# Kernel tuning notes

Hardware: AMD Instinct MI355X
Metric: run time of the kernel (lower is better)

The kernel has to match this reference:

```python
import jax, jax.numpy as jnp
import numpy as np

HID = 1024
RATIO = 4          # compress_ratio
SELECT_K = 512
WINDOW = 256
N_HEADS = 16
SCALE = 1.0 / np.sqrt(HID // N_HEADS)  # 1/sqrt(head_size), head_size=64


def setup_inputs() -> dict:
    key = jax.random.key(0)
    ks = jax.random.split(key, 12)
    std = 0.02
    d = {
        "hidden_states": jax.random.normal(ks[0], (4, 4096, HID), jnp.float32),
        # torch Linear weight [out,in] stored here transposed as [in,out]
        "Wq": jax.random.normal(ks[1], (HID, HID), jnp.float32) * std,
        "bq": jnp.zeros((HID,), jnp.float32),
        "Wk": jax.random.normal(ks[2], (HID, HID), jnp.float32) * std,
        "bk": jnp.zeros((HID,), jnp.float32),
        "Wv": jax.random.normal(ks[3], (HID, HID), jnp.float32) * std,
        "bv": jnp.zeros((HID,), jnp.float32),
        "Wo": jax.random.normal(ks[4], (3 * HID, HID), jnp.float32) * std,
        "bo": jnp.zeros((HID,), jnp.float32),
        "Wg": jax.random.normal(ks[5], (HID, 3), jnp.float32) * std,
        "bg": jnp.zeros((3,), jnp.float32),
        "Wc": jax.random.normal(ks[6], (RATIO * HID, HID), jnp.float32) * std,
        "bc": jnp.zeros((HID,), jnp.float32),
        "Ws": jax.random.normal(ks[7], (HID, 1), jnp.float32) * std,
        "bs": jnp.zeros((1,), jnp.float32),
    }
    return d


def _adjust(t, L):
    cur = t.shape[1]
    if cur < L:
        return jnp.pad(t, ((0, 0), (0, L - cur), (0, 0)))
    return t[:, :L]


def _attend(x, Wq, bq, Wk, bk, Wv, bv):
    # x: [..., T, H]; full single-head attention over axis -2
    q = x @ Wq + bq
    k = x @ Wk + bk
    v = x @ Wv + bv
    s = jnp.einsum('...qd,...kd->...qk', q, k) * SCALE
    p = jax.nn.softmax(s, axis=-1)
    return jnp.einsum('...qk,...kd->...qd', p, v)


def reference(hidden_states, Wq, bq, Wk, bk, Wv, bv, Wo, bo, Wg, bg, Wc, bc, Ws, bs):
    B, L, H = hidden_states.shape

    # --- gates ---
    gates = jax.nn.sigmoid(hidden_states @ Wg + bg)
    gates = gates / (gates.sum(-1, keepdims=True) + 1e-6)

    # --- compress branch: block-compress then full attention over blocks ---
    pad_c = (-L) % RATIO
    xc = jnp.pad(hidden_states, ((0, 0), (0, pad_c), (0, 0)))
    blocks = xc.reshape(B, -1, RATIO * H)
    compressed = blocks @ Wc + bc                      # [B, Lc, H]
    comp_out = _adjust(_attend(compressed, Wq, bq, Wk, bk, Wv, bv), L)

    # --- select branch: top-k token gather then full attention ---
    k_eff = min(SELECT_K, L)
    scores = (hidden_states @ Ws + bs)[..., 0]         # [B, L]
    _, idx = jax.lax.top_k(scores, k_eff)
    idx = jnp.sort(idx, axis=-1)
    selected = jnp.take_along_axis(hidden_states, idx[..., None], axis=1)  # [B, k, H]
    sel_out = _adjust(_attend(selected, Wq, bq, Wk, bk, Wv, bv), L)

    # --- window branch: overlapping sliding windows (stride W/2) ---
    W = min(WINDOW, L)
    pad_w = (-L) % W
    xw = jnp.pad(hidden_states, ((0, 0), (0, pad_w), (0, 0)))
    Lp = xw.shape[1]
    starts = np.arange(0, Lp - W + 1, W // 2)
    widx = starts[:, None] + np.arange(W)              # [nw, W] static
    win = xw[:, widx]                                   # [B, nw, W, H]
    win_ctx = _attend(win, Wq, bq, Wk, bk, Wv, bv)      # [B, nw, W, H]
    win_out = _adjust(win_ctx.reshape(B, -1, H), L)

    # --- gated combine + output projection + residual + layernorm ---
    combined = jnp.concatenate([
        comp_out * gates[..., 0:1],
        sel_out * gates[..., 1:2],
        win_out * gates[..., 2:3],
    ], axis=-1)
    out = combined @ Wo + bo
    out = out * 0.5 + hidden_states * 0.5
    mu = out.mean(-1, keepdims=True)
    var = out.var(-1, keepdims=True)
    return (out - mu) * jax.lax.rsqrt(var + 1e-6)
```

## Files before the change

kernel.cpp:

```cpp
#include <hip/hip_runtime.h>
#include <hip/hip_bf16.h>

typedef __bf16 bf16;
typedef __bf16 bf16x4 __attribute__((ext_vector_type(4)));
typedef __bf16 bf16x8 __attribute__((ext_vector_type(8)));
typedef float floatx4 __attribute__((ext_vector_type(4)));

#define MFMA16(a, b, c) __builtin_amdgcn_mfma_f32_16x16x32_bf16((a), (b), (c), 0, 0, 0)
#define SCALE_F 0.125f

#define GLDS(gp, lp) __builtin_amdgcn_global_load_lds( \
    (const __attribute__((address_space(1))) void*)(gp), \
    (__attribute__((address_space(3))) void*)(lp), 16, 0, 0)

__global__ __launch_bounds__(256) void prep_kernel(const float* __restrict__ Wq, const float* __restrict__ Wk,
                                                   const float* __restrict__ Wv, const float* __restrict__ Wo,
                                                   const float* __restrict__ Wc,
                                                   const float* __restrict__ bq, const float* __restrict__ bk,
                                                   const float* __restrict__ bv,
                                                   bf16* __restrict__ wqkvT, bf16* __restrict__ woT,
                                                   bf16* __restrict__ wcT, float* __restrict__ bqkv) {
    const int z = blockIdx.z;
    const int tx = threadIdx.x, ty = threadIdx.y;
    if (z == 10) {
        int bid = blockIdx.y * 32 + blockIdx.x;
        if (bid < 12) {
            int i = bid * 256 + ty * 32 + tx;
            float v = (i < 1024) ? bq[i] : (i < 2048 ? bk[i - 1024] : bv[i - 2048]);
            bqkv[i] = v;
        }
        return;
    }
    __shared__ float tile[32][33];
    const float* in;
    bf16* out;
    int R;
    if (z < 3)      { in = (z == 0 ? Wq : (z == 1 ? Wk : Wv)); out = wqkvT + (size_t)z * 1048576; R = 1024; }
    else if (z < 6) { in = Wo + (size_t)(z - 3) * 1048576; out = woT + (size_t)(z - 3) * 1048576; R = 1024; }
    else            { in = Wc + (size_t)(z - 6) * 1048576; out = wcT + (z - 6) * 1024; R = 4096; }
    int bx = blockIdx.x * 32, by = blockIdx.y * 32;
#pragma unroll
    for (int i = 0; i < 32; i += 8)
        tile[ty + i][tx] = in[(size_t)(by + ty + i) * 1024 + bx + tx];
    __syncthreads();
#pragma unroll
    for (int i = 0; i < 32; i += 8)
        out[(size_t)(bx + ty + i) * R + by + tx] = (bf16)tile[tx][ty + i];
}

__global__ __launch_bounds__(256) void gates_scores_kernel(const float* __restrict__ x,
                                                           const float* __restrict__ Wg, const float* __restrict__ bg,
                                                           const float* __restrict__ Ws, const float* __restrict__ bs,
                                                           float* __restrict__ gates, float* __restrict__ scores,
                                                           bf16* __restrict__ xb) {
    int row = blockIdx.x * 4 + (threadIdx.x >> 6);
    int lane = threadIdx.x & 63;
    const float* xr = x + (size_t)row * 1024 + lane * 16;
    float g0 = 0.f, g1 = 0.f, g2 = 0.f;
    double sc = 0.0;
    bf16x8 xo0, xo1;
#pragma unroll
    for (int i = 0; i < 16; i++) {
        float xv = xr[i];
        if (i < 8) xo0[i] = (bf16)xv; else xo1[i - 8] = (bf16)xv;
        int k = lane * 16 + i;
        g0 += xv * Wg[k * 3 + 0];
        g1 += xv * Wg[k * 3 + 1];
        g2 += xv * Wg[k * 3 + 2];
        sc += (double)(xv * Ws[k]);
    }
    bf16* xbp = xb + (size_t)row * 1024 + lane * 16;
    *(bf16x8*)xbp = xo0;
    *(bf16x8*)(xbp + 8) = xo1;
    for (int off = 1; off < 64; off <<= 1) {
        g0 += __shfl_xor(g0, off);
        g1 += __shfl_xor(g1, off);
        g2 += __shfl_xor(g2, off);
        sc += __shfl_xor(sc, off);
    }
    if (lane == 0) {
        g0 = 1.0f / (1.0f + __expf(-(g0 + bg[0])));
        g1 = 1.0f / (1.0f + __expf(-(g1 + bg[1])));
        g2 = 1.0f / (1.0f + __expf(-(g2 + bg[2])));
        float den = g0 + g1 + g2 + 1e-6f;
        gates[(size_t)row * 3 + 0] = g0 / den;
        gates[(size_t)row * 3 + 1] = g1 / den;
        gates[(size_t)row * 3 + 2] = g2 / den;
        scores[row] = (float)(sc + (double)bs[0]);
    }
}

__global__ __launch_bounds__(256) void rank_kernel(const float* __restrict__ scores, int* __restrict__ rankP) {
    __shared__ float s[1024];
    const int b = blockIdx.z, jc = blockIdx.y;
    const int i = blockIdx.x * 256 + threadIdx.x;
    const float* sb = scores + b * 4096;
    ((float4*)s)[threadIdx.x] = ((const float4*)(sb + jc * 1024))[threadIdx.x];
    __syncthreads();
    const float si = sb[i];
    const int jbase = jc * 1024;
    int cnt = 0;
#pragma unroll 4
    for (int jj = 0; jj < 1024; jj += 4) {
        float4 v = *(const float4*)(s + jj);
        int j0 = jbase + jj;
        cnt += (v.x > si) || (v.x == si && (j0 + 0) < i);
        cnt += (v.y > si) || (v.y == si && (j0 + 1) < i);
        cnt += (v.z > si) || (v.z == si && (j0 + 2) < i);
        cnt += (v.w > si) || (v.w == si && (j0 + 3) < i);
    }
    rankP[jc * 16384 + b * 4096 + i] = cnt;
}

__global__ __launch_bounds__(1024) void select_kernel(const int* __restrict__ rankP, int* __restrict__ sidx) {
    __shared__ int psum[1024];
    int b = blockIdx.x, t = threadIdx.x;
    const int* rb = rankP + b * 4096;
    int f[4];
#pragma unroll
    for (int k = 0; k < 4; k++) {
        int idx = 4 * t + k;
        int r = rb[idx] + rb[16384 + idx] + rb[32768 + idx] + rb[49152 + idx];
        f[k] = r < 512;
    }
    psum[t] = f[0] + f[1] + f[2] + f[3];
    __syncthreads();
    for (int off = 1; off < 1024; off <<= 1) {
        int u = (t >= off) ? psum[t - off] : 0;
        __syncthreads();
        psum[t] += u;
        __syncthreads();
    }
    int pos = t ? psum[t - 1] : 0;
    int* ob = sidx + b * 512;
    if (f[0]) ob[pos++] = 4 * t + 0;
    if (f[1]) ob[pos++] = 4 * t + 1;
    if (f[2]) ob[pos++] = 4 * t + 2;
    if (f[3]) ob[pos++] = 4 * t + 3;
}

__global__ __launch_bounds__(256) void gather_kernel(const bf16* __restrict__ Qf, const bf16* __restrict__ Kf,
                                                     const bf16* __restrict__ Vf, const int* __restrict__ sidx,
                                                     bf16* __restrict__ sq, bf16* __restrict__ sk,
                                                     bf16* __restrict__ sv) {
    int e = blockIdx.x * 256 + threadIdx.x;
    int col = (e & 127) * 8;
    int i = (e >> 7) & 511;
    int b = e >> 16;
    int src = b * 4096 + (sidx[b * 512 + i] & 4095);
    size_t so = (size_t)src * 1024 + col;
    size_t dofs = (size_t)(b * 512 + i) * 1024 + col;
    *(float4*)(sq + dofs) = *(const float4*)(Qf + so);
    *(float4*)(sk + dofs) = *(const float4*)(Kf + so);
    *(float4*)(sv + dofs) = *(const float4*)(Vf + so);
}

__global__ __launch_bounds__(256) void addcvt4_kernel(const float* __restrict__ P0, const float* __restrict__ P1,
                                                      const float* __restrict__ P2, const float* __restrict__ P3,
                                                      const float* __restrict__ bc, bf16* __restrict__ outp) {
    int i = blockIdx.x * 256 + threadIdx.x;
    float4 a = ((const float4*)P0)[i];
    float4 b = ((const float4*)P1)[i];
    float4 c = ((const float4*)P2)[i];
    float4 d = ((const float4*)P3)[i];
    int col = (i << 2) & 1023;
    bf16x4 o;
    o[0] = (bf16)(a.x + b.x + c.x + d.x + bc[col + 0]);
    o[1] = (bf16)(a.y + b.y + c.y + d.y + bc[col + 1]);
    o[2] = (bf16)(a.z + b.z + c.z + d.z + bc[col + 2]);
    o[3] = (bf16)(a.w + b.w + c.w + d.w + bc[col + 3]);
    *(bf16x4*)(outp + ((size_t)i << 2)) = o;
}

template <bool F32OUT, bool ACC, bool REMAP>
__device__ __forceinline__ void gemm3_body(int nt, int mt, int zh, int zl, bf16* sA, bf16* sB,
                                           const bf16* __restrict__ A, const bf16* __restrict__ Bt,
                                           void* __restrict__ Cv, const float* __restrict__ bias, int biasz,
                                           int K, int lda, int ldb, int ldc,
                                           size_t sAhi, size_t sAlo, size_t sBhi, size_t sBlo,
                                           size_t sChi, size_t sClo, int mpbA, int mpbC) {
    const int t = threadIdx.x;
    const int lane = t & 63, quad = lane >> 4, l16 = lane & 15;
    const int wv = t >> 6, wm = wv >> 1, wn = wv & 1;
    A  += (size_t)zh * sAhi + (size_t)zl * sAlo;
    Bt += (size_t)zh * sBhi + (size_t)zl * sBlo;
    const size_t cofs = (size_t)zh * sChi + (size_t)zl * sClo;

    floatx4 acc[4][4] = {};

    const bf16* Ap = A + (size_t)(mt * 128 + (t >> 2)) * lda + (t & 3) * 8;
    const bf16* Bp = Bt + (size_t)(nt * 128 + (t >> 2)) * ldb + (t & 3) * 8;
    const size_t rA = (size_t)64 * lda, rB = (size_t)64 * ldb;
    bf16* lA0 = sA + wv * 512;
    bf16* lA1 = sA + 2048 + wv * 512;
    bf16* lB0 = sB + wv * 512;
    bf16* lB1 = sB + 2048 + wv * 512;

    for (int k0 = 0; k0 < K; k0 += 32) {
        __syncthreads();
        GLDS(Ap + k0,      lA0);
        GLDS(Ap + rA + k0, lA1);
        GLDS(Bp + k0,      lB0);
        GLDS(Bp + rB + k0, lB1);
        __syncthreads();
        bf16x8 af[4], bfr[4];
#pragma unroll
        for (int i = 0; i < 4; i++) af[i] = *(const bf16x8*)(sA + (wm * 64 + i * 16 + l16) * 32 + quad * 8);
#pragma unroll
        for (int j = 0; j < 4; j++) bfr[j] = *(const bf16x8*)(sB + (wn * 64 + j * 16 + l16) * 32 + quad * 8);
#pragma unroll
        for (int i = 0; i < 4; i++)
#pragma unroll
            for (int j = 0; j < 4; j++) acc[i][j] = MFMA16(af[i], bfr[j], acc[i][j]);
    }

#pragma unroll
    for (int i = 0; i < 4; i++) {
        int gr0 = mt * 128 + wm * 64 + i * 16 + quad * 4;
#pragma unroll
        for (int j = 0; j < 4; j++) {
            int gc = nt * 128 + wn * 64 + j * 16 + l16;
            float bvl = bias ? bias[zl * biasz + gc] : 0.0f;
#pragma unroll
            for (int r = 0; r < 4; r++) {
                int row = gr0 + r;
                size_t crow = REMAP ? ((size_t)(row / mpbA) * mpbC + (row % mpbA)) : (size_t)row;
                size_t off = cofs + crow * ldc + gc;
                float v = acc[i][j][r] + bvl;
                if constexpr (F32OUT) {
                    float* Cf = (float*)Cv;
                    if constexpr (ACC) v += Cf[off];
                    Cf[off] = v;
                } else {
                    bf16* Cb = (bf16*)Cv;
                    if constexpr (ACC) v += (float)Cb[off];
                    Cb[off] = (bf16)v;
                }
            }
        }
    }
}

template <bool NZF, bool F32OUT, bool ACC, bool REMAP>
__global__ __launch_bounds__(256) void gemm3(const bf16* __restrict__ A, const bf16* __restrict__ Bt,
                                             void* __restrict__ Cv, const float* __restrict__ bias, int biasz,
                                             int K, int lda, int ldb, int ldc, int zdiv,
                                             size_t sAhi, size_t sAlo, size_t sBhi, size_t sBlo,
                                             size_t sChi, size_t sClo, int mpbA, int mpbC) {
    __shared__ float4 smA[512], smB[512];
    const int mt = blockIdx.y;
    int nt, zh, zl;
    if constexpr (NZF) {
        zh = blockIdx.z;
        zl = blockIdx.x / zdiv;
        nt = blockIdx.x - zl * zdiv;
    } else {
        nt = blockIdx.x;
        int z = blockIdx.z;
        zh = z / zdiv;
        zl = z - zh * zdiv;
    }
    gemm3_body<F32OUT, ACC, REMAP>(nt, mt, zh, zl, (bf16*)smA, (bf16*)smB,
                                   A, Bt, Cv, bias, biasz, K, lda, ldb, ldc,
                                   sAhi, sAlo, sBhi, sBlo, sChi, sClo, mpbA, mpbC);
}

template <bool F32OUT>
__global__ __launch_bounds__(256) void gemm3_pair(int nzA, int nxB, int nyB,
        const bf16* __restrict__ A1, const bf16* __restrict__ B1, void* __restrict__ C1,
        int K1, int lda1, int ldb1, int ldc1, size_t sAhi1, size_t sBhi1, size_t sChi1,
        const bf16* __restrict__ A2, const bf16* __restrict__ B2, void* __restrict__ C2,
        int K2, int lda2, int ldb2, int ldc2, size_t sAhi2, size_t sBhi2, size_t sChi2) {
    __shared__ float4 smA[512], smB[512];
    if ((int)blockIdx.z < nzA) {
        gemm3_body<F32OUT, false, false>(blockIdx.x, blockIdx.y, blockIdx.z, 0, (bf16*)smA, (bf16*)smB,
                                         A1, B1, C1, nullptr, 0, K1, lda1, ldb1, ldc1,
                                         sAhi1, 0, sBhi1, 0, sChi1, 0, 1, 1);
    } else {
        if ((int)blockIdx.x >= nxB || (int)blockIdx.y >= nyB) return;
        gemm3_body<F32OUT, false, false>(blockIdx.x, blockIdx.y, blockIdx.z - nzA, 0, (bf16*)smA, (bf16*)smB,
                                         A2, B2, C2, nullptr, 0, K2, lda2, ldb2, ldc2,
                                         sAhi2, 0, sBhi2, 0, sChi2, 0, 1, 1);
    }
}

#define BARx()   asm volatile("s_barrier" ::: "memory")
#define LGKM0()  asm volatile("s_waitcnt lgkmcnt(0)" ::: "memory")
#define VMC6()   asm volatile("s_waitcnt vmcnt(6)" ::: "memory")

#define LD_A(bsel, qm) { \
    const bf16* _p = lds + (bsel) * 32768 + (((qm) << 7) + (wm << 6) + l16) * 64; \
    _Pragma("unroll") \
    for (int m = 0; m < 4; m++) { \
        a[m][0] = *(const bf16x8*)(_p + (m << 10) + cg0); \
        a[m][1] = *(const bf16x8*)(_p + (m << 10) + cg1); \
    } }

#define LD_B(bsel, qn) { \
    const bf16* _p = lds + (bsel) * 32768 + 16384 + (((qn) << 7) + (wn << 5) + l16) * 64; \
    _Pragma("unroll") \
    for (int n = 0; n < 2; n++) { \
        b[qn][n][0] = *(const bf16x8*)(_p + (n << 10) + cg0); \
        b[qn][n][1] = *(const bf16x8*)(_p + (n << 10) + cg1); \
    } }

#define ST_A(bsel, h, ko) { \
    bf16* _d = lds + (bsel) * 32768 + (((h) << 7) + (wv << 3)) * 64; \
    const bf16* _g = Ab + (size_t)((h) << 7) * lda + (ko); \
    GLDS(_g, _d); \
    GLDS(_g + ((size_t)lda << 6), _d + 4096); }

#define ST_B(bsel, h, ko) { \
    bf16* _d = lds + (bsel) * 32768 + 16384 + (((h) << 7) + (wv << 3)) * 64; \
    const bf16* _g = Bb + (size_t)((h) << 7) * ldb + (ko); \
    GLDS(_g, _d); \
    GLDS(_g + ((size_t)ldb << 6), _d + 4096); }

#define PH_MMA(qm, qn) { \
    __builtin_amdgcn_s_setprio(1); \
    _Pragma("unroll") \
    for (int kk = 0; kk < 2; kk++) \
    _Pragma("unroll") \
    for (int m = 0; m < 4; m++) \
    _Pragma("unroll") \
    for (int n = 0; n < 2; n++) \
        acc[qm][qn][m][n] = MFMA16(a[m][kk], b[qn][n][kk], acc[qm][qn][m][n]); \
    __builtin_amdgcn_s_setprio(0); }

template <bool NZF, bool F32OUT, bool ACC, bool REMAP>
__global__ __launch_bounds__(512, 2) void gemm256(const bf16* __restrict__ A, const bf16* __restrict__ Bt,
                                                  void* __restrict__ Cv, const float* __restrict__ bias, int biasz,
                                                  int K, int lda, int ldb, int ldc, int zdiv,
                                                  size_t sAhi, size_t sAlo, size_t sBhi, size_t sBlo,
                                                  size_t sChi, size_t sClo, int mpbA, int mpbC) {
    __shared__ float4 ldsv[8192];
    bf16* lds = (bf16*)ldsv;
    const int t = threadIdx.x;
    const int lane = t & 63, quad = lane >> 4, l16 = lane & 15;
    const int wv = t >> 6, wm = wv >> 2, wn = wv & 3;

    const int gx = gridDim.x;
    int lin = blockIdx.x + gx * blockIdx.y;
    const int chunk = (gx * gridDim.y) >> 3;
    lin = (lin & 7) * chunk + (lin >> 3);
    const int bx = lin % gx;
    const int mt = lin / gx;

    int nt, zh, zl;
    if constexpr (NZF) {
        zh = blockIdx.z;
        zl = bx / zdiv;
        nt = bx - zl * zdiv;
    } else {
        nt = bx;
        int z = blockIdx.z;
        zh = z / zdiv;
        zl = z - zh * zdiv;
    }
    A  += (size_t)zh * sAhi + (size_t)zl * sAlo;
    Bt += (size_t)zh * sBhi + (size_t)zl * sBlo;
    const size_t cofs = (size_t)zh * sChi + (size_t)zl * sClo;

    const int srow = (wv << 3) + (lane >> 3);
    const int scol = (((lane & 7) ^ ((lane >> 3) & 7)) << 3);
    const bf16* Ab = A + (size_t)(mt * 256 + srow) * lda + scol;
    const bf16* Bb = Bt + (size_t)(nt * 256 + srow) * ldb + scol;
    const int swz = l16 & 7;
    const int cg0 = ((quad ^ swz) << 3);
    const int cg1 = (((4 | quad) ^ swz) << 3);

    floatx4 acc[2][2][4][2] = {};
    bf16x8 a[4][2], b[2][2][2];

    const int NT = K >> 6;
    ST_A(0, 0, 0);  ST_B(0, 0, 0);  ST_B(0, 1, 0);  ST_A(0, 1, 0);
    ST_A(1, 0, 64); ST_B(1, 0, 64); ST_B(1, 1, 64); ST_A(1, 1, 64);
    VMC6();
    BARx();

#pragma unroll 1
    for (int it = 0; it < (NT >> 1); ++it) {
        const int kt = it << 1;
        const int ko2 = ((kt + 2 < NT) ? kt + 2 : NT - 1) << 6;
        const int ko3 = ((kt + 3 < NT) ? kt + 3 : NT - 1) << 6;
        LD_B(0, 0); LD_A(0, 0);
        PH_MMA(0, 0);
        LGKM0(); BARx();
        LD_B(0, 1);
        ST_A(0, 0, ko2);
        PH_MMA(0, 1);
        LGKM0(); BARx();
        LD_A(0, 1);
        ST_B(0, 0, ko2);
        PH_MMA(1, 1);
        LGKM0(); BARx();
        ST_B(0, 1, ko2);
        PH_MMA(1, 0);
        VMC6(); BARx();
        LD_B(1, 0); LD_A(1, 0);
        ST_A(0, 1, ko2);
        PH_MMA(0, 0);
        LGKM0(); BARx();
        LD_B(1, 1);
        ST_A(1, 0, ko3);
        PH_MMA(0, 1);
        LGKM0(); BARx();
        LD_A(1, 1);
        ST_B(1, 0, ko3);
        PH_MMA(1, 1);
        LGKM0(); BARx();
        ST_B(1, 1, ko3);
        ST_A(1, 1, ko3);
        PH_MMA(1, 0);
        VMC6(); BARx();
    }

    asm volatile("s_waitcnt vmcnt(0)" ::: "memory");
    BARx();

    if constexpr (!ACC && !REMAP) {
        const int STE = F32OUT ? 260 : 264;
        float* ldsf = (float*)ldsv;
        bf16* ldsh = (bf16*)ldsv;
#pragma unroll
        for (int qm = 0; qm < 2; qm++)
#pragma unroll
        for (int mh = 0; mh < 2; mh++) {
#pragma unroll
            for (int qn = 0; qn < 2; qn++)
#pragma unroll
            for (int n = 0; n < 2; n++) {
                const int ccol = qn * 128 + wn * 32 + n * 16 + l16;
                const float bvl = bias ? bias[zl * biasz + nt * 256 + ccol] : 0.0f;
#pragma unroll
                for (int mp = 0; mp < 2; mp++) {
                    const int lr0 = wm * 32 + mp * 16 + quad * 4;
#pragma unroll
                    for (int r = 0; r < 4; r++) {
                        float v = acc[qm][qn][mh * 2 + mp][n][r] + bvl;
                        if constexpr (F32OUT) ldsf[(lr0 + r) * STE + ccol] = v;
                        else                  ldsh[(lr0 + r) * STE + ccol] = (bf16)v;
                    }
                }
            }
            LGKM0(); BARx();
            if constexpr (F32OUT) {
                float* Cf = (float*)Cv;
#pragma unroll
                for (int i = 0; i < 8; i++) {
                    int idx = i * 512 + t;
                    int row = idx >> 6, c4 = (idx & 63) << 2;
                    float4 vv = *(float4*)(ldsf + row * STE + c4);
                    int grow = mt * 256 + qm * 128 + ((row >> 5) << 6) + mh * 32 + (row & 31);
                    *(float4*)(Cf + cofs + (size_t)grow * ldc + nt * 256 + c4) = vv;
                }
            } else {
                bf16* Cb = (bf16*)Cv;
#pragma unroll
                for (int i = 0; i < 4; i++) {
                    int idx = i * 512 + t;
                    int row = idx >> 5, c8 = (idx & 31) << 3;
                    float4 vv = *(float4*)(ldsh + row * STE + c8);
                    int grow = mt * 256 + qm * 128 + ((row >> 5) << 6) + mh * 32 + (row & 31);
                    *(float4*)(Cb + cofs + (size_t)grow * ldc + nt * 256 + c8) = vv;
                }
            }
            LGKM0(); BARx();
        }
    } else {
#pragma unroll
        for (int qm = 0; qm < 2; qm++)
#pragma unroll
        for (int m = 0; m < 4; m++) {
            int gr0 = mt * 256 + qm * 128 + wm * 64 + m * 16 + quad * 4;
#pragma unroll
            for (int qn = 0; qn < 2; qn++)
#pragma unroll
            for (int n = 0; n < 2; n++) {
                int gc = nt * 256 + qn * 128 + wn * 32 + n * 16 + l16;
                float bvl = bias ? bias[zl * biasz + gc] : 0.0f;
#pragma unroll
                for (int r = 0; r < 4; r++) {
                    int row = gr0 + r;
                    size_t crow = REMAP ? ((size_t)(row / mpbA) * mpbC + (row % mpbA)) : (size_t)row;
                    size_t off = cofs + crow * ldc + gc;
                    float v = acc[qm][qn][m][n][r] + bvl;
                    if constexpr (F32OUT) {
                        float* Cf = (float*)Cv;
                        if constexpr (ACC) v += Cf[off];
                        Cf[off] = v;
                    } else {
                        bf16* Cb = (bf16*)Cv;
                        if constexpr (ACC) v += (float)Cb[off];
                        Cb[off] = (bf16)v;
                    }
                }
            }
        }
    }
}

#undef LD_A
#undef LD_B
#undef ST_A
#undef ST_B
#undef PH_MMA

__device__ __forceinline__ void sm_body(const float* __restrict__ srow, bf16* __restrict__ prow,
                                        int npt, float gate, float* red) {
    const int t = threadIdx.x;
    float v[4];
    float m = -1e30f;
    for (int i = 0; i < npt; i++) { v[i] = srow[t + (i << 8)] * SCALE_F; m = fmaxf(m, v[i]); }
    for (int off = 1; off < 64; off <<= 1) m = fmaxf(m, __shfl_xor(m, off));
    const int wvv = t >> 6, lane = t & 63;
    if (lane == 0) red[wvv] = m;
    __syncthreads();
    m = fmaxf(fmaxf(red[0], red[1]), fmaxf(red[2], red[3]));
    float e[4], s = 0.f;
    for (int i = 0; i < npt; i++) { e[i] = __expf(v[i] - m); s += e[i]; }
    for (int off = 1; off < 64; off <<= 1) s += __shfl_xor(s, off);
    if (lane == 0) red[4 + wvv] = s;
    __syncthreads();
    s = red[4] + red[5] + red[6] + red[7];
    const float fac = gate / s;
    for (int i = 0; i < npt; i++) prow[t + (i << 8)] = (bf16)(e[i] * fac);
}

__device__ __forceinline__ void tp_body(const bf16* __restrict__ tin, bf16* __restrict__ tout,
                                        int TR, int TC, int tb, bf16 (*tile)[33]) {
    const int t = threadIdx.x;
    int bx = (tb & 31) * 32, by = (tb >> 5) * 32;
    int tx = t & 31, ty = t >> 5;
#pragma unroll
    for (int i = 0; i < 32; i += 8)
        tile[ty + i][tx] = tin[(size_t)(by + ty + i) * TC + bx + tx];
    __syncthreads();
#pragma unroll
    for (int i = 0; i < 32; i += 8)
        tout[(size_t)(bx + ty + i) * TR + by + tx] = tile[tx][ty + i];
}

__global__ __launch_bounds__(256) void smtb_win_kernel(const float* __restrict__ S, bf16* __restrict__ P,
                                                       const float* __restrict__ gates, int nsm,
                                                       const bf16* __restrict__ tin, bf16* __restrict__ tout) {
    __shared__ float red[8];
    __shared__ bf16 tile[32][33];
    if ((int)blockIdx.x >= nsm) {
        tp_body(tin, tout, 16384, 1024, blockIdx.x - nsm, tile);
        return;
    }
    const int row = blockIdx.x;
    int zz = row >> 8;
    int gpos = (zz / 16) * 4096 + (zz % 16) * 256 + (row & 255);
    sm_body(S + (size_t)row * 256, P + (size_t)row * 256, 1, gates[gpos * 3 + 2], red);
}

__global__ __launch_bounds__(256) void smtb2_kernel(const float* __restrict__ S0, bf16* __restrict__ P0,
                                                    const float* __restrict__ S1, bf16* __restrict__ P1,
                                                    const float* __restrict__ gates,
                                                    const bf16* __restrict__ cv, bf16* __restrict__ cvT,
                                                    const bf16* __restrict__ sv, bf16* __restrict__ svT) {
    __shared__ float red[8];
    __shared__ bf16 tile[32][33];
    const int i = blockIdx.x;
    if (i < 4096) {
        int gpos = (i >> 10) * 4096 + (i & 1023);
        sm_body(S0 + (size_t)i * 1024, P0 + (size_t)i * 1024, 4, gates[gpos * 3 + 0], red);
    } else if (i < 8192) {
        tp_body(cv, cvT, 4096, 1024, i - 4096, tile);
    } else if (i < 10240) {
        int row = i - 8192;
        int gpos = (row >> 9) * 4096 + (row & 511);
        sm_body(S1 + (size_t)row * 512, P1 + (size_t)row * 512, 2, gates[gpos * 3 + 1], red);
    } else {
        tp_body(sv, svT, 2048, 1024, i - 10240, tile);
    }
}

__global__ __launch_bounds__(256) void ln_kernel(float* __restrict__ acc, const float* __restrict__ x) {
    __shared__ float red[8];
    int row = blockIdx.x, t = threadIdx.x;
    float4 a = ((const float4*)(acc + (size_t)row * 1024))[t];
    float4 xv = ((const float4*)(x + (size_t)row * 1024))[t];
    float y[4];
    y[0] = 0.5f * a.x + 0.5f * xv.x;
    y[1] = 0.5f * a.y + 0.5f * xv.y;
    y[2] = 0.5f * a.z + 0.5f * xv.z;
    y[3] = 0.5f * a.w + 0.5f * xv.w;
    float s = 0.f, s2 = 0.f;
#pragma unroll
    for (int i = 0; i < 4; i++) { s += y[i]; s2 += y[i] * y[i]; }
    for (int off = 1; off < 64; off <<= 1) { s += __shfl_xor(s, off); s2 += __shfl_xor(s2, off); }
    int wvv = t >> 6, lane = t & 63;
    if (lane == 0) { red[wvv] = s; red[4 + wvv] = s2; }
    __syncthreads();
    s = red[0] + red[1] + red[2] + red[3];
    s2 = red[4] + red[5] + red[6] + red[7];
    float mu = s * (1.0f / 1024.0f);
    float var = s2 * (1.0f / 1024.0f) - mu * mu;
    float rs = rsqrtf(var + 1e-6f);
    float4 o;
    o.x = (y[0] - mu) * rs;
    o.y = (y[1] - mu) * rs;
    o.z = (y[2] - mu) * rs;
    o.w = (y[3] - mu) * rs;
    ((float4*)(acc + (size_t)row * 1024))[t] = o;
}

extern "C" void kernel_launch(void* const* d_in, const int* in_sizes, int n_in,
                              void* d_out, int out_size, void* d_ws, size_t ws_size,
                              hipStream_t stream) {
    (void)in_sizes; (void)n_in; (void)out_size; (void)ws_size;
    const float* x  = (const float*)d_in[0];
    const float* Wq = (const float*)d_in[1];
    const float* bq = (const float*)d_in[2];
    const float* Wk = (const float*)d_in[3];
    const float* bk = (const float*)d_in[4];
    const float* Wv = (const float*)d_in[5];
    const float* bv = (const float*)d_in[6];
    const float* Wo = (const float*)d_in[7];
    const float* bo = (const float*)d_in[8];
    const float* Wg = (const float*)d_in[9];
    const float* bg = (const float*)d_in[10];
    const float* Wc = (const float*)d_in[11];
    const float* bc = (const float*)d_in[12];
    const float* Ws = (const float*)d_in[13];
    const float* bs = (const float*)d_in[14];
    float* out = (float*)d_out;

    char* w = (char*)d_ws;
    const size_t MB = 1024 * 1024;
    bf16* xb    = (bf16*)(w + 0 * MB);
    bf16* Pwin  = (bf16*)(w + 0 * MB);
    bf16* cq    = (bf16*)(w + 0 * MB);
    bf16* ck    = (bf16*)(w + 8 * MB);
    bf16* cv    = (bf16*)(w + 16 * MB);
    bf16* Pcomp = (bf16*)(w + 24 * MB);
    bf16* Psel  = (bf16*)(w + 4 * MB);
    bf16* sel_o = (bf16*)(w + 6 * MB);
    bf16* qf    = (bf16*)(w + 32 * MB);
    bf16* vfT   = (bf16*)(w + 32 * MB);
    bf16* kf    = (bf16*)(w + 64 * MB);
    bf16* win_o = (bf16*)(w + 64 * MB);
    bf16* vf    = (bf16*)(w + 96 * MB);
    bf16* comp  = (bf16*)(w + 128 * MB);
    float* compP = (float*)(w + 32 * MB);
    int* rankP = (int*)(w + 96 * MB);
    bf16* cvT = (bf16*)(w + 96 * MB);
    float* SselN = (float*)(w + 104 * MB);
    float* Swin  = (float*)(w + 136 * MB);
    float* Scomp = (float*)(w + 136 * MB);
    bf16* comp_o = (bf16*)(w + 144 * MB);
    bf16* wqkvT = (bf16*)(w + 152 * MB);
    bf16* wcT   = (bf16*)(w + 158 * MB);
    bf16* woT0  = (bf16*)(w + 166 * MB);
    bf16* woT1  = (bf16*)(w + 168 * MB);
    bf16* woT2  = (bf16*)(w + 170 * MB);
    bf16* sq    = (bf16*)(w + 172 * MB);
    bf16* sk    = (bf16*)(w + 176 * MB);
    bf16* sv    = (bf16*)(w + 180 * MB);
    bf16* svT   = (bf16*)(w + 184 * MB);
    float* bqkv    = (float*)(w + 188 * MB);
    float* gatesF  = bqkv + 3072;
    float* scoresF = gatesF + 49152;
    int*   sidx    = (int*)(scoresF + 16384);

    dim3 tb(32, 8);

    gates_scores_kernel<<<4096, 256, 0, stream>>>(x, Wg, bg, Ws, bs, gatesF, scoresF, xb);
    prep_kernel<<<dim3(32, 32, 11), tb, 0, stream>>>(Wq, Wk, Wv, Wo, Wc, bq, bk, bv, wqkvT, woT0, wcT, bqkv);
    rank_kernel<<<dim3(16, 4, 4), 256, 0, stream>>>(scoresF, rankP);
    select_kernel<<<4, 1024, 0, stream>>>(rankP, sidx);

    gemm256<false,true,false,false><<<dim3(4, 16, 4), 512, 0, stream>>>(
        xb, wcT, compP, nullptr, 0, 1024, 4096, 4096, 1024, 1,
        (size_t)1024, 0, (size_t)1024, 0, (size_t)4194304, 0, 1, 1);
    addcvt4_kernel<<<4096, 256, 0, stream>>>(compP, compP + (size_t)4194304,
                                             compP + (size_t)8388608, compP + (size_t)12582912, bc, comp);

    gemm256<true,false,false,false><<<dim3(12, 64, 1), 512, 0, stream>>>(
        xb, wqkvT, qf, bqkv, 1024, 1024, 1024, 1024, 1024, 4,
        0, 0, 0, (size_t)1048576, 0, (size_t)16777216, 1, 1);

    gather_kernel<<<1024, 256, 0, stream>>>(qf, kf, vf, sidx, sq, sk, sv);

    gemm3<false,true,false,false><<<dim3(2, 2, 64), 256, 0, stream>>>(
        qf, kf, Swin, nullptr, 0, 1024, 1024, 1024, 256, 16,
        (size_t)4194304, (size_t)131072, (size_t)4194304, (size_t)131072, (size_t)1048576, (size_t)65536, 1, 1);
    smtb_win_kernel<<<32768, 256, 0, stream>>>(Swin, Pwin, gatesF, 16384, vf, vfT);
    gemm3<false,false,false,false><<<dim3(8, 2, 64), 256, 0, stream>>>(
        Pwin, vfT, win_o, nullptr, 0, 256, 256, 16384, 1024, 16,
        (size_t)1048576, (size_t)65536, (size_t)4096, (size_t)128, (size_t)4194304, (size_t)262144, 1, 1);
    gemm256<false,true,false,false><<<dim3(4, 64, 1), 512, 0, stream>>>(
        win_o, woT2, out, bo, 0, 1024, 1024, 1024, 1024, 1, 0, 0, 0, 0, 0, 0, 1, 1);

    gemm256<true,false,false,false><<<dim3(12, 16, 1), 512, 0, stream>>>(
        comp, wqkvT, cq, bqkv, 1024, 1024, 1024, 1024, 1024, 4,
        0, 0, 0, (size_t)1048576, 0, (size_t)4194304, 1, 1);

    gemm3_pair<true><<<dim3(8, 8, 8), 256, 0, stream>>>(4, 4, 4,
        cq, ck, Scomp, 1024, 1024, 1024, 1024, (size_t)1048576, (size_t)1048576, (size_t)1048576,
        sq, sk, SselN, 1024, 1024, 1024, 512, (size_t)524288, (size_t)524288, (size_t)262144);

    smtb2_kernel<<<12288, 256, 0, stream>>>(Scomp, Pcomp, SselN, Psel, gatesF, cv, cvT, sv, svT);

    gemm3_pair<false><<<dim3(8, 8, 8), 256, 0, stream>>>(4, 8, 4,
        Pcomp, cvT, comp_o, 1024, 1024, 4096, 1024, (size_t)1048576, (size_t)1024, (size_t)1048576,
        Psel, svT, sel_o, 512, 512, 2048, 1024, (size_t)262144, (size_t)512, (size_t)524288);

    gemm3<false,true,true,true><<<dim3(8, 32, 1), 256, 0, stream>>>(
        comp_o, woT0, out, nullptr, 0, 1024, 1024, 1024, 1024, 1, 0, 0, 0, 0, 0, 0, 1024, 4096);
    gemm3<false,true,true,true><<<dim3(8, 16, 1), 256, 0, stream>>>(
        sel_o, woT1, out, nullptr, 0, 1024, 1024, 1024, 1024, 1, 0, 0, 0, 0, 0, 0, 512, 4096);

    ln_kernel<<<16384, 256, 0, stream>>>(out, x);
}
```

Measured before the change: 733.7 us.

## Merge three output-projection GEMMs into one launch and fold partial sums into layernorm

Replaces the separate window, compress and select output-projection GEMMs (one gemm256 plus two accumulating gemm3 calls) with a single gemm3_tri launch. The three problems are spread across the grid z dimension, and the compress and select partial products go to separate fp32 buffers. The layernorm kernel now adds those partial products for the rows they cover before the residual and normalisation. This removes launch overhead and the read-modify-write accumulation into the output, at the cost of extra scratch buffers and using the 256-thread gemm3 tile instead of the 512-thread gemm256 for the large window projection.

Result: faster. 681.2 us (-7.2%).

```diff
diff --git a/kernel.cpp b/kernel.cpp
--- a/kernel.cpp
+++ b/kernel.cpp
@@ -281,6 +281,29 @@
         gemm3_body<F32OUT, false, false>(blockIdx.x, blockIdx.y, blockIdx.z - nzA, 0, (bf16*)smA, (bf16*)smB,
                                          A2, B2, C2, nullptr, 0, K2, lda2, ldb2, ldc2,
                                          sAhi2, 0, sBhi2, 0, sChi2, 0, 1, 1);
+    }
+}
+
+__global__ __launch_bounds__(256) void gemm3_tri(int ny1, int ny2,
+        const bf16* __restrict__ A0, const bf16* __restrict__ B0, float* __restrict__ C0,
+        const float* __restrict__ bias0,
+        const bf16* __restrict__ A1, const bf16* __restrict__ B1, float* __restrict__ C1,
+        const bf16* __restrict__ A2, const bf16* __restrict__ B2, float* __restrict__ C2) {
+    __shared__ float4 smA[512], smB[512];
+    if (blockIdx.z == 0) {
+        gemm3_body<true, false, false>(blockIdx.x, blockIdx.y, 0, 0, (bf16*)smA, (bf16*)smB,
+                                       A0, B0, C0, bias0, 0, 1024, 1024, 1024, 1024,
+                                       0, 0, 0, 0, 0, 0, 1, 1);
+    } else if (blockIdx.z == 1) {
+        if ((int)blockIdx.y >= ny1) return;
+        gemm3_body<true, false, false>(blockIdx.x, blockIdx.y, 0, 0, (bf16*)smA, (bf16*)smB,
+                                       A1, B1, C1, nullptr, 0, 1024, 1024, 1024, 1024,
+                                       0, 0, 0, 0, 0, 0, 1, 1);
+    } else {
+        if ((int)blockIdx.y >= ny2) return;
+        gemm3_body<true, false, false>(blockIdx.x, blockIdx.y, 0, 0, (bf16*)smA, (bf16*)smB,
+                                       A2, B2, C2, nullptr, 0, 1024, 1024, 1024, 1024,
+                                       0, 0, 0, 0, 0, 0, 1, 1);
     }
 }
 
@@ -578,10 +601,20 @@
     }
 }
 
-__global__ __launch_bounds__(256) void ln_kernel(float* __restrict__ acc, const float* __restrict__ x) {
+__global__ __launch_bounds__(256) void ln_kernel(float* __restrict__ acc, const float* __restrict__ x,
+                                                 const float* __restrict__ compPr, const float* __restrict__ selPr) {
     __shared__ float red[8];
     int row = blockIdx.x, t = threadIdx.x;
+    int b = row >> 12, idx = row & 4095;
     float4 a = ((const float4*)(acc + (size_t)row * 1024))[t];
+    if (idx < 1024) {
+        float4 c = ((const float4*)(compPr + (size_t)(b * 1024 + idx) * 1024))[t];
+        a.x += c.x; a.y += c.y; a.z += c.z; a.w += c.w;
+    }
+    if (idx < 512) {
+        float4 s4 = ((const float4*)(selPr + (size_t)(b * 512 + idx) * 1024))[t];
+        a.x += s4.x; a.y += s4.y; a.z += s4.z; a.w += s4.w;
+    }
     float4 xv = ((const float4*)(x + (size_t)row * 1024))[t];
     float y[4];
     y[0] = 0.5f * a.x + 0.5f * xv.x;
@@ -646,6 +679,8 @@
     bf16* vf    = (bf16*)(w + 96 * MB);
     bf16* comp  = (bf16*)(w + 128 * MB);
     float* compP = (float*)(w + 32 * MB);
+    float* compPr = (float*)(w + 32 * MB);
+    float* selPr  = (float*)(w + 48 * MB);
     int* rankP = (int*)(w + 96 * MB);
     bf16* cvT = (bf16*)(w + 96 * MB);
     float* SselN = (float*)(w + 104 * MB);
@@ -692,8 +727,6 @@
     gemm3<false,false,false,false><<<dim3(8, 2, 64), 256, 0, stream>>>(
         Pwin, vfT, win_o, nullptr, 0, 256, 256, 16384, 1024, 16,
         (size_t)1048576, (size_t)65536, (size_t)4096, (size_t)128, (size_t)4194304, (size_t)262144, 1, 1);
-    gemm256<false,true,false,false><<<dim3(4, 64, 1), 512, 0, stream>>>(
-        win_o, woT2, out, bo, 0, 1024, 1024, 1024, 1024, 1, 0, 0, 0, 0, 0, 0, 1, 1);
 
     gemm256<true,false,false,false><<<dim3(12, 16, 1), 512, 0, stream>>>(
         comp, wqkvT, cq, bqkv, 1024, 1024, 1024, 1024, 1024, 4,
@@ -709,10 +742,10 @@
         Pcomp, cvT, comp_o, 1024, 1024, 4096, 1024, (size_t)1048576, (size_t)1024, (size_t)1048576,
         Psel, svT, sel_o, 512, 512, 2048, 1024, (size_t)262144, (size_t)512, (size_t)524288);
 
-    gemm3<false,true,true,true><<<dim3(8, 32, 1), 256, 0, stream>>>(
-        comp_o, woT0, out, nullptr, 0, 1024, 1024, 1024, 1024, 1, 0, 0, 0, 0, 0, 0, 1024, 4096);
-    gemm3<false,true,true,true><<<dim3(8, 16, 1), 256, 0, stream>>>(
-        sel_o, woT1, out, nullptr, 0, 1024, 1024, 1024, 1024, 1, 0, 0, 0, 0, 0, 0, 512, 4096);
-
-    ln_kernel<<<16384, 256, 0, stream>>>(out, x);
-}
+    gemm3_tri<<<dim3(8, 128, 3), 256, 0, stream>>>(32, 16,
+        win_o, woT2, out, bo,
+        comp_o, woT0, compPr,
+        sel_o, woT1, selPr);
+
+    ln_kernel<<<16384, 256, 0, stream>>>(out, x, compPr, selPr);
+}
```

## Fuse window QK^T with gather and merge output-projection GEMMs into one launch

Applied to the files above, without the earlier changes.

Merges the windowed QK^T GEMM and the selected-token gather into a single launch, with block ranges dispatched by block index. The two accumulate-into-out GEMMs for the compress and select output projections become one paired launch. That paired launch writes to separate fp32 buffers, and the LayerNorm kernel adds those partials back in for the relevant rows. The aim is to cut launch count and let independent work overlap, at the cost of extra fp32 partial traffic read inside the LayerNorm.

After: 685.9 us. 6.5% less time.

```diff
diff --git a/kernel.cpp b/kernel.cpp
--- a/kernel.cpp
+++ b/kernel.cpp
@@ -139,22 +139,6 @@
     if (f[3]) ob[pos++] = 4 * t + 3;
 }
 
-__global__ __launch_bounds__(256) void gather_kernel(const bf16* __restrict__ Qf, const bf16* __restrict__ Kf,
-                                                     const bf16* __restrict__ Vf, const int* __restrict__ sidx,
-                                                     bf16* __restrict__ sq, bf16* __restrict__ sk,
-                                                     bf16* __restrict__ sv) {
-    int e = blockIdx.x * 256 + threadIdx.x;
-    int col = (e & 127) * 8;
-    int i = (e >> 7) & 511;
-    int b = e >> 16;
-    int src = b * 4096 + (sidx[b * 512 + i] & 4095);
-    size_t so = (size_t)src * 1024 + col;
-    size_t dofs = (size_t)(b * 512 + i) * 1024 + col;
-    *(float4*)(sq + dofs) = *(const float4*)(Qf + so);
-    *(float4*)(sk + dofs) = *(const float4*)(Kf + so);
-    *(float4*)(sv + dofs) = *(const float4*)(Vf + so);
-}
-
 __global__ __launch_bounds__(256) void addcvt4_kernel(const float* __restrict__ P0, const float* __restrict__ P1,
                                                       const float* __restrict__ P2, const float* __restrict__ P3,
                                                       const float* __restrict__ bc, bf16* __restrict__ outp) {
@@ -284,6 +268,33 @@
     }
 }
 
+__global__ __launch_bounds__(256) void winqkt_gather_kernel(
+        const bf16* __restrict__ qf, const bf16* __restrict__ kf, float* __restrict__ Swin,
+        const bf16* __restrict__ Vf, const int* __restrict__ sidx,
+        bf16* __restrict__ sq, bf16* __restrict__ sk, bf16* __restrict__ sv) {
+    if ((int)blockIdx.x < 256) {
+        __shared__ float4 smA[512], smB[512];
+        int b = blockIdx.x;
+        int nt = b & 1, mt = (b >> 1) & 1, zz = b >> 2;
+        int zh = zz >> 4, zl = zz & 15;
+        gemm3_body<true, false, false>(nt, mt, zh, zl, (bf16*)smA, (bf16*)smB,
+                                       qf, kf, Swin, nullptr, 0, 1024, 1024, 1024, 256,
+                                       (size_t)4194304, (size_t)131072, (size_t)4194304, (size_t)131072,
+                                       (size_t)1048576, (size_t)65536, 1, 1);
+        return;
+    }
+    int e = (blockIdx.x - 256) * 256 + threadIdx.x;
+    int col = (e & 127) * 8;
+    int i = (e >> 7) & 511;
+    int b = e >> 16;
+    int src = b * 4096 + (sidx[b * 512 + i] & 4095);
+    size_t so = (size_t)src * 1024 + col;
+    size_t dofs = (size_t)(b * 512 + i) * 1024 + col;
+    *(float4*)(sq + dofs) = *(const float4*)(qf + so);
+    *(float4*)(sk + dofs) = *(const float4*)(kf + so);
+    *(float4*)(sv + dofs) = *(const float4*)(Vf + so);
+}
+
 #define BARx()   asm volatile("s_barrier" ::: "memory")
 #define LGKM0()  asm volatile("s_waitcnt lgkmcnt(0)" ::: "memory")
 #define VMC6()   asm volatile("s_waitcnt vmcnt(6)" ::: "memory")
@@ -327,36 +338,18 @@
         acc[qm][qn][m][n] = MFMA16(a[m][kk], b[qn][n][kk], acc[qm][qn][m][n]); \
     __builtin_amdgcn_s_setprio(0); }
 
-template <bool NZF, bool F32OUT, bool ACC, bool REMAP>
-__global__ __launch_bounds__(512, 2) void gemm256(const bf16* __restrict__ A, const bf16* __restrict__ Bt,
-                                                  void* __restrict__ Cv, const float* __restrict__ bias, int biasz,
-                                                  int K, int lda, int ldb, int ldc, int zdiv,
-                                                  size_t sAhi, size_t sAlo, size_t sBhi, size_t sBlo,
-                                                  size_t sChi, size_t sClo, int mpbA, int mpbC) {
-    __shared__ float4 ldsv[8192];
+template <bool F32OUT, bool ACC, bool REMAP>
+__device__ __forceinline__ void gemm256_body(int mt, int nt, int zh, int zl, float4* ldsv,
+        const bf16* __restrict__ A, const bf16* __restrict__ Bt,
+        void* __restrict__ Cv, const float* __restrict__ bias, int biasz,
+        int K, int lda, int ldb, int ldc,
+        size_t sAhi, size_t sAlo, size_t sBhi, size_t sBlo,
+        size_t sChi, size_t sClo, int mpbA, int mpbC) {
     bf16* lds = (bf16*)ldsv;
     const int t = threadIdx.x;
     const int lane = t & 63, quad = lane >> 4, l16 = lane & 15;
     const int wv = t >> 6, wm = wv >> 2, wn = wv & 3;
 
-    const int gx = gridDim.x;
-    int lin = blockIdx.x + gx * blockIdx.y;
-    const int chunk = (gx * gridDim.y) >> 3;
-    lin = (lin & 7) * chunk + (lin >> 3);
-    const int bx = lin % gx;
-    const int mt = lin / gx;
-
-    int nt, zh, zl;
-    if constexpr (NZF) {
-        zh = blockIdx.z;
-        zl = bx / zdiv;
-        nt = bx - zl * zdiv;
-    } else {
-        nt = bx;
-        int z = blockIdx.z;
-        zh = z / zdiv;
-        zl = z - zh * zdiv;
-    }
     A  += (size_t)zh * sAhi + (size_t)zl * sAlo;
     Bt += (size_t)zh * sBhi + (size_t)zl * sBlo;
     const size_t cofs = (size_t)zh * sChi + (size_t)zl * sClo;
@@ -500,6 +493,35 @@
     }
 }
 
+template <bool NZF, bool F32OUT, bool ACC, bool REMAP>
+__global__ __launch_bounds__(512, 2) void gemm256(const bf16* __restrict__ A, const bf16* __restrict__ Bt,
+                                                  void* __restrict__ Cv, const float* __restrict__ bias, int biasz,
+                                                  int K, int lda, int ldb, int ldc, int zdiv,
+                                                  size_t sAhi, size_t sAlo, size_t sBhi, size_t sBlo,
+                                                  size_t sChi, size_t sClo, int mpbA, int mpbC) {
+    __shared__ float4 ldsv[8192];
+    const int gx = gridDim.x;
+    int lin = blockIdx.x + gx * blockIdx.y;
+    const int chunk = (gx * gridDim.y) >> 3;
+    lin = (lin & 7) * chunk + (lin >> 3);
+    const int bx = lin % gx;
+    const int mt = lin / gx;
+
+    int nt, zh, zl;
+    if constexpr (NZF) {
+        zh = blockIdx.z;
+        zl = bx / zdiv;
+        nt = bx - zl * zdiv;
+    } else {
+        nt = bx;
+        int z = blockIdx.z;
+        zh = z / zdiv;
+        zl = z - zh * zdiv;
+    }
+    gemm256_body<F32OUT, ACC, REMAP>(mt, nt, zh, zl, ldsv, A, Bt, Cv, bias, biasz,
+                                     K, lda, ldb, ldc, sAhi, sAlo, sBhi, sBlo, sChi, sClo, mpbA, mpbC);
+}
+
 #undef LD_A
 #undef LD_B
 #undef ST_A
@@ -578,10 +600,20 @@
     }
 }
 
-__global__ __launch_bounds__(256) void ln_kernel(float* __restrict__ acc, const float* __restrict__ x) {
+__global__ __launch_bounds__(256) void ln_kernel(float* __restrict__ acc, const float* __restrict__ x,
+                                                 const float* __restrict__ compPr, const float* __restrict__ selPr) {
     __shared__ float red[8];
     int row = blockIdx.x, t = threadIdx.x;
+    int b = row >> 12, idx = row & 4095;
     float4 a = ((const float4*)(acc + (size_t)row * 1024))[t];
+    if (idx < 1024) {
+        float4 c = ((const float4*)(compPr + (size_t)(b * 1024 + idx) * 1024))[t];
+        a.x += c.x; a.y += c.y; a.z += c.z; a.w += c.w;
+    }
+    if (idx < 512) {
+        float4 s4 = ((const float4*)(selPr + (size_t)(b * 512 + idx) * 1024))[t];
+        a.x += s4.x; a.y += s4.y; a.z += s4.z; a.w += s4.w;
+    }
     float4 xv = ((const float4*)(x + (size_t)row * 1024))[t];
     float y[4];
     y[0] = 0.5f * a.x + 0.5f * xv.x;
@@ -646,6 +678,8 @@
     bf16* vf    = (bf16*)(w + 96 * MB);
     bf16* comp  = (bf16*)(w + 128 * MB);
     float* compP = (float*)(w + 32 * MB);
+    float* compPr = (float*)(w + 32 * MB);
+    float* selPr  = (float*)(w + 48 * MB);
     int* rankP = (int*)(w + 96 * MB);
     bf16* cvT = (bf16*)(w + 96 * MB);
     float* SselN = (float*)(w + 104 * MB);
@@ -683,11 +717,8 @@
         xb, wqkvT, qf, bqkv, 1024, 1024, 1024, 1024, 1024, 4,
         0, 0, 0, (size_t)1048576, 0, (size_t)16777216, 1, 1);
 
-    gather_kernel<<<1024, 256, 0, stream>>>(qf, kf, vf, sidx, sq, sk, sv);
-
-    gemm3<false,true,false,false><<<dim3(2, 2, 64), 256, 0, stream>>>(
-        qf, kf, Swin, nullptr, 0, 1024, 1024, 1024, 256, 16,
-        (size_t)4194304, (size_t)131072, (size_t)4194304, (size_t)131072, (size_t)1048576, (size_t)65536, 1, 1);
+    winqkt_gather_kernel<<<1280, 256, 0, stream>>>(qf, kf, Swin, vf, sidx, sq, sk, sv);
+
     smtb_win_kernel<<<32768, 256, 0, stream>>>(Swin, Pwin, gatesF, 16384, vf, vfT);
     gemm3<false,false,false,false><<<dim3(8, 2, 64), 256, 0, stream>>>(
         Pwin, vfT, win_o, nullptr, 0, 256, 256, 16384, 1024, 16,
@@ -709,10 +740,9 @@
         Pcomp, cvT, comp_o, 1024, 1024, 4096, 1024, (size_t)1048576, (size_t)1024, (size_t)1048576,
         Psel, svT, sel_o, 512, 512, 2048, 1024, (size_t)262144, (size_t)512, (size_t)524288);
 
-    gemm3<false,true,true,true><<<dim3(8, 32, 1), 256, 0, stream>>>(
-        comp_o, woT0, out, nullptr, 0, 1024, 1024, 1024, 1024, 1, 0, 0, 0, 0, 0, 0, 1024, 4096);
-    gemm3<false,true,true,true><<<dim3(8, 16, 1), 256, 0, stream>>>(
-        sel_o, woT1, out, nullptr, 0, 1024, 1024, 1024, 1024, 1, 0, 0, 0, 0, 0, 0, 512, 4096);
-
-    ln_kernel<<<16384, 256, 0, stream>>>(out, x);
-}
+    gemm3_pair<true><<<dim3(8, 32, 2), 256, 0, stream>>>(1, 8, 16,
+        comp_o, woT0, compPr, 1024, 1024, 1024, 1024, 0, 0, 0,
+        sel_o, woT1, selPr, 1024, 1024, 1024, 1024, 0, 0, 0);
+
+    ln_kernel<<<16384, 256, 0, stream>>>(out, x, compPr, selPr);
+}
```
